# Optimization experiments

Hardware: AMD Instinct MI355X
Metric: run time of the kernel (lower is better)

The kernel has to match this reference:

```python
import jax, jax.numpy as jnp
import numpy as np

IMG_H, IMG_W = 800.0, 1280.0
STRIDE = 16
SCALE = 1.0 / STRIDE
P, S = 14, 1              # pooler resolution, sampling ratio
NUM_CLASSES = 80
BBOX_W = (10.0, 10.0, 5.0, 5.0)
SCORE_TH, NMS_TH, MAX_DET, IOU_TH = 0.05, 0.5, 100, 0.5
SCALE_CLAMP = float(np.log(1000.0 / 16.0))


def _make_boxes(key, n_img, n_box):
    k1, k2, k3, k4 = jax.random.split(key, 4)
    x1 = jax.random.uniform(k1, (n_img, n_box)) * (IMG_W - 64.0)
    y1 = jax.random.uniform(k2, (n_img, n_box)) * (IMG_H - 64.0)
    w = jax.random.uniform(k3, (n_img, n_box)) * 300.0 + 16.0
    h = jax.random.uniform(k4, (n_img, n_box)) * 300.0 + 16.0
    x2 = jnp.minimum(x1 + w, IMG_W)
    y2 = jnp.minimum(y1 + h, IMG_H)
    return jnp.stack([x1, y1, x2, y2], axis=-1)


def setup_inputs() -> dict:
    key = jax.random.key(0)
    ks = jax.random.split(key, 6)
    features = jax.random.normal(ks[0], (2, 50, 80, 1024), dtype=jnp.float32)
    proposals = _make_boxes(ks[1], 2, 256)
    gt_boxes = _make_boxes(ks[2], 2, 64)
    gt_classes = jax.random.randint(ks[3], (2, 64), 0, NUM_CLASSES)
    W_cls = jax.random.normal(ks[4], (1024, NUM_CLASSES + 1), dtype=jnp.float32) * 0.01
    b_cls = jnp.zeros((NUM_CLASSES + 1,), jnp.float32)
    W_box = jax.random.normal(ks[5], (1024, 4), dtype=jnp.float32) * 0.01
    b_box = jnp.zeros((4,), jnp.float32)
    return {"features": features, "proposals": proposals, "gt_boxes": gt_boxes,
            "gt_classes": gt_classes, "W_cls": W_cls, "b_cls": b_cls,
            "W_box": W_box, "b_box": b_box}


def pairwise_iou(a, b):
    # a: [G,4], b: [R,4], boxes as (x1,y1,x2,y2) -> [G,R]
    area_a = (a[:, 2] - a[:, 0]) * (a[:, 3] - a[:, 1])
    area_b = (b[:, 2] - b[:, 0]) * (b[:, 3] - b[:, 1])
    lt = jnp.maximum(a[:, None, :2], b[None, :, :2])
    rb = jnp.minimum(a[:, None, 2:], b[None, :, 2:])
    wh = jnp.clip(rb - lt, 0.0)
    inter = wh[..., 0] * wh[..., 1]
    return inter / jnp.maximum(area_a[:, None] + area_b[None, :] - inter, 1e-9)


def roi_align_one(feat, boxes):
    # feat: [H,W,C], boxes: [R,4] in image coords -> pooled [R,P,P,C]
    H, W, C = feat.shape
    b = boxes * SCALE
    x1, y1, x2, y2 = b[:, 0], b[:, 1], b[:, 2], b[:, 3]
    off = (jnp.arange(S, dtype=feat.dtype) + 0.5) / S       # [S]
    grid = jnp.arange(P, dtype=feat.dtype)                   # [P]
    bh = ((y2 - y1) / P)[:, None, None]
    bw = ((x2 - x1) / P)[:, None, None]
    # aligned RoIAlign sample coords (half-pixel offset)
    gy = y1[:, None, None] + (grid[None, :, None] + off[None, None, :]) * bh - 0.5  # [R,P,S]
    gx = x1[:, None, None] + (grid[None, :, None] + off[None, None, :]) * bw - 0.5
    gy = jnp.clip(gy, 0.0, H - 1.0)
    gx = jnp.clip(gx, 0.0, W - 1.0)
    y0 = jnp.floor(gy); x0 = jnp.floor(gx)
    y0i = y0.astype(jnp.int32); x0i = x0.astype(jnp.int32)
    y1i = jnp.minimum(y0i + 1, H - 1); x1i = jnp.minimum(x0i + 1, W - 1)
    ly = gy - y0; lx = gx - x0

    def g(yi, xi):  # cross-product gather -> [R,P,S,P,S,C]
        return feat[yi[:, :, :, None, None], xi[:, None, None, :, :]]

    wy0 = (1.0 - ly)[:, :, :, None, None, None]; wy1 = ly[:, :, :, None, None, None]
    wx0 = (1.0 - lx)[:, None, None, :, :, None]; wx1 = lx[:, None, None, :, :, None]
    val = wy0 * (wx0 * g(y0i, x0i) + wx1 * g(y0i, x1i)) \
        + wy1 * (wx0 * g(y1i, x0i) + wx1 * g(y1i, x1i))
    return val.mean(axis=(2, 4))  # average sampling points per bin -> [R,P,P,C]


def decode_boxes(deltas, boxes):
    wx, wy, ww, wh = BBOX_W
    widths = boxes[..., 2] - boxes[..., 0]
    heights = boxes[..., 3] - boxes[..., 1]
    ctr_x = boxes[..., 0] + 0.5 * widths
    ctr_y = boxes[..., 1] + 0.5 * heights
    dx = deltas[..., 0] / wx
    dy = deltas[..., 1] / wy
    dw = jnp.minimum(deltas[..., 2] / ww, SCALE_CLAMP)
    dh = jnp.minimum(deltas[..., 3] / wh, SCALE_CLAMP)
    pcx = dx * widths + ctr_x
    pcy = dy * heights + ctr_y
    pw = jnp.exp(dw) * widths
    ph = jnp.exp(dh) * heights
    out = jnp.stack([pcx - 0.5 * pw, pcy - 0.5 * ph, pcx + 0.5 * pw, pcy + 0.5 * ph], axis=-1)
    lim = jnp.array([IMG_W, IMG_H, IMG_W, IMG_H], out.dtype)
    return jnp.clip(out, 0.0, lim)


def nms_keep(boxes, scores):
    # greedy class-agnostic NMS, fixed-size keep mask [R]
    R = scores.shape[0]
    order = jnp.argsort(-scores)
    sb = boxes[order]
    iou = pairwise_iou(sb, sb)
    idx = jnp.arange(R)

    def body(i, keep):
        suppressed = jnp.any((idx < i) & keep & (iou[:, i] > NMS_TH))
        return keep.at[i].set(jnp.logical_not(suppressed))

    keep_sorted = jax.lax.fori_loop(0, R, body, jnp.ones((R,), bool))
    return jnp.zeros((R,), bool).at[order].set(keep_sorted)


def reference(features, proposals, gt_boxes, gt_classes, W_cls, b_cls, W_box, b_box):
    N, R = proposals.shape[:2]
    # --- proposal <-> gt matching (training-side labeling) ---
    iou_m = jax.vmap(pairwise_iou)(gt_boxes, proposals)          # [N,G,R]
    matched_vals = iou_m.max(axis=1)
    matched_idxs = iou_m.argmax(axis=1)                          # [N,R]
    match_labels = (matched_vals >= IOU_TH).astype(jnp.int32)    # [N,R] fg=1/bg=0
    # --- RoIAlign pooling on the single C4 feature map ---
    pooled = jax.vmap(roi_align_one)(features, proposals)        # [N,R,P,P,C]
    feat_vec = pooled.mean(axis=(2, 3))                          # res5 surrogate global avg -> [N,R,C]
    # --- box predictor ---
    scores_all = jax.nn.softmax(feat_vec @ W_cls + b_cls, axis=-1)
    fg_scores = scores_all[..., :NUM_CLASSES].max(axis=-1)       # drop background column
    deltas = feat_vec @ W_box + b_box
    boxes = decode_boxes(deltas, proposals)                      # [N,R,4]
    # --- score threshold + NMS + top-k ---
    keep = jax.vmap(nms_keep)(boxes, fg_scores) & (fg_scores > SCORE_TH)
    masked = jnp.where(keep, fg_scores, -jnp.inf)
    rank = jnp.argsort(jnp.argsort(-masked, axis=-1), axis=-1)
    keep = keep & (rank < MAX_DET)
    det = jnp.concatenate([boxes, fg_scores[..., None], keep.astype(boxes.dtype)[..., None]], axis=-1)
    return det, matched_idxs, match_labels
```

## Files before the change

kernel.cpp:

```cpp
#include <hip/hip_runtime.h>
#include <math.h>

#define N_IMG 2
#define R_PROP 256
#define G_GT 64
#define C_CH 1024
#define FH 50
#define FW 80
#define P_POOL 14
#define NCLS 80
#define IMG_W_F 1280.0f
#define IMG_H_F 800.0f
#define SCALE_F 0.0625f
#define SCORE_TH_F 0.05f
#define NMS_TH_F 0.5f
#define IOU_TH_F 0.5f
#define MAX_DET_I 100
#define SCALE_CLAMP_F 4.135166556742356f

__global__ __launch_bounds__(512) void prep_kernel(
    const float* __restrict__ proposals,
    const float* __restrict__ gt_boxes,
    int* __restrict__ perm,
    float* __restrict__ out_idx,
    float* __restrict__ out_lbl) {
  const int t = threadIdx.x;
  const int n = t >> 8;
  __shared__ float cy[N_IMG * R_PROP];
  const float* pb = proposals + (size_t)t * 4;
  float bx1 = pb[0], by1 = pb[1], bx2 = pb[2], by2 = pb[3];
  cy[t] = by1 + by2;
  __syncthreads();

  {
    float my = cy[t];
    int rk = 0;
    const int base = n * R_PROP;
#pragma unroll 8
    for (int j = base; j < base + R_PROP; ++j) {
      float cj = cy[j];
      rk += (cj < my) || (cj == my && j < t);
    }
    perm[base + rk] = t & 255;
  }

  {
    float area_b = (bx2 - bx1) * (by2 - by1);
    float best = -1.0f;
    int bidx = 0;
    const float* gt = gt_boxes + (size_t)n * G_GT * 4;
#pragma unroll 4
    for (int g = 0; g < G_GT; ++g) {
      float gx1 = gt[g * 4 + 0], gy1 = gt[g * 4 + 1];
      float gx2 = gt[g * 4 + 2], gy2 = gt[g * 4 + 3];
      float area_a = (gx2 - gx1) * (gy2 - gy1);
      float ix1 = fmaxf(gx1, bx1), iy1 = fmaxf(gy1, by1);
      float ix2 = fminf(gx2, bx2), iy2 = fminf(gy2, by2);
      float iw = fmaxf(ix2 - ix1, 0.0f), ih = fmaxf(iy2 - iy1, 0.0f);
      float inter = iw * ih;
      float iou = inter / fmaxf(area_a + area_b - inter, 1e-9f);
      if (iou > best) { best = iou; bidx = g; }
    }
    out_idx[t] = (float)bidx;
    out_lbl[t] = (best >= IOU_TH_F) ? 1.0f : 0.0f;
  }
}

__global__ __launch_bounds__(1024) void roihead_kernel(
    const float* __restrict__ features,
    const float* __restrict__ proposals,
    const int* __restrict__ perm,
    const float* __restrict__ W_cls,
    const float* __restrict__ W_box,
    float* __restrict__ part) {
  const int b = blockIdx.x;
  const int xcd = b & 7;
  const int slot = b >> 3;
  const int n = xcd >> 2;
  const int band = xcd & 3;
  const int h = slot & 1;
  const int blk = n * R_PROP + perm[n * R_PROP + band * 64 + (slot >> 1)];

  const float* feat = features + (size_t)n * (FH * FW * C_CH) + h * (C_CH / 2);
  const int t = threadIdx.x;
  const int c4 = t & 127;
  const int g = t >> 7;

  __shared__ float s_Wy[FH];
  __shared__ float s_Wx[FW];
  __shared__ int s_b[4];
  __shared__ float4 s_red[7][128];
  __shared__ __align__(16) float sf[C_CH / 2];
  __shared__ float s_part[12][85];

  if (t < FH) s_Wy[t] = 0.0f;
  if (t >= 128 && t < 128 + FW) s_Wx[t - 128] = 0.0f;
  __syncthreads();

  if (t < 2 * P_POOL) {
    const float* pb = proposals + (size_t)blk * 4;
    bool isY = t < P_POOL;
    int i = isY ? t : t - P_POOL;
    float lo = isY ? pb[1] : pb[0];
    float hi = isY ? pb[3] : pb[2];
    float limit = isY ? (float)(FH - 1) : (float)(FW - 1);
    float b1 = lo * SCALE_F, b2 = hi * SCALE_F;
    float bs = (b2 - b1) * (1.0f / P_POOL);
    float gg = b1 + ((float)i + 0.5f) * bs - 0.5f;
    gg = fminf(fmaxf(gg, 0.0f), limit);
    float fl = floorf(gg);
    int i0 = (int)fl;
    int i1 = min(i0 + 1, (int)limit);
    float l = gg - fl;
    if (isY) {
      atomicAdd(&s_Wy[i0], 1.0f - l);
      atomicAdd(&s_Wy[i1], l);
      if (i == 0) s_b[0] = i0;
      if (i == P_POOL - 1) s_b[1] = i1;
    } else {
      atomicAdd(&s_Wx[i0], 1.0f - l);
      atomicAdd(&s_Wx[i1], l);
      if (i == 0) s_b[2] = i0;
      if (i == P_POOL - 1) s_b[3] = i1;
    }
  }
  __syncthreads();

  {
    const int ylo = s_b[0], yhi = s_b[1], xlo = s_b[2], xhi = s_b[3];
    float4 acc = make_float4(0.f, 0.f, 0.f, 0.f);
    for (int y = ylo + g; y <= yhi; y += 8) {
      float wy = s_Wy[y];
      const float4* row = (const float4*)(feat + (size_t)y * (FW * C_CH)) + c4;
#pragma unroll 8
      for (int x = xlo; x <= xhi; ++x) {
        float w = wy * s_Wx[x];
        float4 f = row[x * (C_CH / 4)];
        acc.x += w * f.x;
        acc.y += w * f.y;
        acc.z += w * f.z;
        acc.w += w * f.w;
      }
    }
    if (g > 0) s_red[g - 1][c4] = acc;
    __syncthreads();
    if (g == 0) {
      const float inv = 1.0f / (float)(P_POOL * P_POOL);
#pragma unroll
      for (int p = 0; p < 7; ++p) {
        float4 a = s_red[p][c4];
        acc.x += a.x; acc.y += a.y; acc.z += a.z; acc.w += a.w;
      }
      ((float4*)sf)[c4] =
          make_float4(acc.x * inv, acc.y * inv, acc.z * inv, acc.w * inv);
    }
    __syncthreads();
  }

  const int kq = t / 85;
  const int j = t - kq * 85;
  if (kq < 12) {
    float acc = 0.0f;
    const int kbase = h * (C_CH / 2);
    if (j < 81) {
      const float* __restrict__ w = W_cls + (size_t)kbase * 81 + j;
#pragma unroll 8
      for (int k = kq; k < C_CH / 2; k += 12) acc += sf[k] * w[k * 81];
    } else {
      const float* __restrict__ w = W_box + (size_t)kbase * 4 + (j - 81);
#pragma unroll 8
      for (int k = kq; k < C_CH / 2; k += 12) acc += sf[k] * w[k * 4];
    }
    s_part[kq][j] = acc;
  }
  __syncthreads();

  if (t < 85) {
    float acc = 0.0f;
#pragma unroll
    for (int p = 0; p < 12; ++p) acc += s_part[p][t];
    part[(size_t)blk * 170 + h * 85 + t] = acc;
  }
}

__global__ __launch_bounds__(128) void finalize_kernel(
    const float* __restrict__ part,
    const float* __restrict__ proposals,
    const float* __restrict__ b_cls,
    const float* __restrict__ b_box,
    float* __restrict__ boxes_dec,
    float* __restrict__ scores) {
  const int blk = blockIdx.x;
  const int t = threadIdx.x;
  __shared__ float sl[85];
  __shared__ float s_red[8];

  const float* pp = part + (size_t)blk * 170;
  if (t < 85) {
    float bias = (t < 81) ? b_cls[t] : b_box[t - 81];
    sl[t] = pp[t] + pp[85 + t] + bias;
  }
  __syncthreads();

  {
    float xm = (t < 81) ? sl[t] : -INFINITY;
    float xf = (t < NCLS) ? sl[t] : -INFINITY;
#pragma unroll
    for (int off = 32; off; off >>= 1) {
      xm = fmaxf(xm, __shfl_down(xm, off, 64));
      xf = fmaxf(xf, __shfl_down(xf, off, 64));
    }
    if ((t & 63) == 0) { s_red[t >> 6] = xm; s_red[2 + (t >> 6)] = xf; }
  }
  __syncthreads();
  const float m = fmaxf(s_red[0], s_red[1]);
  {
    float xs = (t < 81) ? expf(sl[t] - m) : 0.0f;
#pragma unroll
    for (int off = 32; off; off >>= 1) xs += __shfl_down(xs, off, 64);
    if ((t & 63) == 0) s_red[4 + (t >> 6)] = xs;
  }
  __syncthreads();

  if (t == 0) {
    float sum = s_red[4] + s_red[5];
    float fgm = fmaxf(s_red[2], s_red[3]);
    scores[blk] = expf(fgm - m) / sum;

    const float* pb = proposals + (size_t)blk * 4;
    float w = pb[2] - pb[0], h = pb[3] - pb[1];
    float cx = pb[0] + 0.5f * w, cy = pb[1] + 0.5f * h;
    float dx = sl[81] * 0.1f;
    float dy = sl[82] * 0.1f;
    float dw = fminf(sl[83] * 0.2f, SCALE_CLAMP_F);
    float dh = fminf(sl[84] * 0.2f, SCALE_CLAMP_F);
    float pcx = dx * w + cx, pcy = dy * h + cy;
    float pw = expf(dw) * w, ph = expf(dh) * h;
    float ox1 = fminf(fmaxf(pcx - 0.5f * pw, 0.0f), IMG_W_F);
    float oy1 = fminf(fmaxf(pcy - 0.5f * ph, 0.0f), IMG_H_F);
    float ox2 = fminf(fmaxf(pcx + 0.5f * pw, 0.0f), IMG_W_F);
    float oy2 = fminf(fmaxf(pcy + 0.5f * ph, 0.0f), IMG_H_F);
    float* bd = boxes_dec + (size_t)blk * 4;
    bd[0] = ox1; bd[1] = oy1; bd[2] = ox2; bd[3] = oy2;
  }
}

__global__ __launch_bounds__(1024) void nms_kernel(
    const float* __restrict__ boxes_dec,
    const float* __restrict__ scores,
    float* __restrict__ det) {
  const int n = blockIdx.x;
  const int u = threadIdx.x;
  const int i = u & 255;
  const int q = u >> 8;
  const int j40 = q * 16;

  __shared__ __align__(16) float ss[R_PROP];
  __shared__ float4 sbs[R_PROP];
  __shared__ int s_part[4 * R_PROP];
  __shared__ int s_rank[R_PROP];
  __shared__ __align__(16) unsigned long long s_mask[R_PROP * 4];
  __shared__ unsigned long long s_keep[4];
  __shared__ __align__(16) float sm[R_PROP];

  float4 myb;
  float mys;
  if (q == 0) {
    myb = ((const float4*)boxes_dec)[n * R_PROP + i];
    mys = scores[n * R_PROP + i];
    ss[i] = mys;
  }
  __syncthreads();

  {
    float s = ss[i];
    int cnt = 0;
#pragma unroll
    for (int j4 = j40; j4 < j40 + 16; ++j4) {
      float4 v = ((const float4*)ss)[j4];
      int jb = j4 * 4;
      cnt += (v.x > s) || (v.x == s && jb + 0 < i);
      cnt += (v.y > s) || (v.y == s && jb + 1 < i);
      cnt += (v.z > s) || (v.z == s && jb + 2 < i);
      cnt += (v.w > s) || (v.w == s && jb + 3 < i);
    }
    s_part[q * R_PROP + i] = cnt;
  }
  __syncthreads();
  if (q == 0) {
    int rk = s_part[i] + s_part[R_PROP + i] + s_part[2 * R_PROP + i] +
             s_part[3 * R_PROP + i];
    s_rank[i] = rk;
    sbs[rk] = myb;
  }
  __syncthreads();

  {
    float4 bi = sbs[i];
    float area_i = (bi.z - bi.x) * (bi.w - bi.y);
    unsigned long long m = 0;
    const int j0 = q * 64;
#pragma unroll 8
    for (int jj = 0; jj < 64; ++jj) {
      float4 bj = sbs[j0 + jj];
      float area_j = (bj.z - bj.x) * (bj.w - bj.y);
      float ix1 = fmaxf(bi.x, bj.x), iy1 = fmaxf(bi.y, bj.y);
      float ix2 = fminf(bi.z, bj.z), iy2 = fminf(bi.w, bj.w);
      float iw = fmaxf(ix2 - ix1, 0.0f), ih = fmaxf(iy2 - iy1, 0.0f);
      float inter = iw * ih;
      float iou = inter / fmaxf(area_i + area_j - inter, 1e-9f);
      m |= (iou > NMS_TH_F) ? (1ull << jj) : 0ull;
    }
    s_mask[i * 4 + q] = m;
  }
  __syncthreads();

  if (u == 0) {
    unsigned long long K0 = ~0ull, K1 = ~0ull, K2 = ~0ull, K3 = ~0ull;
#pragma unroll 16
    for (int b = 1; b < 64; ++b) {
      unsigned long long m0 = s_mask[(size_t)b * 4 + 0];
      unsigned long long sup = m0 & K0 & ((1ull << b) - 1ull);
      K0 = sup ? (K0 & ~(1ull << b)) : K0;
    }
#pragma unroll 16
    for (int b = 0; b < 64; ++b) {
      const unsigned long long* mi = &s_mask[(size_t)(64 + b) * 4];
      unsigned long long m0 = mi[0], m1 = mi[1];
      unsigned long long sup = (m0 & K0) | (m1 & K1 & ((1ull << b) - 1ull));
      K1 = sup ? (K1 & ~(1ull << b)) : K1;
    }
#pragma unroll 16
    for (int b = 0; b < 64; ++b) {
      const unsigned long long* mi = &s_mask[(size_t)(128 + b) * 4];
      unsigned long long m0 = mi[0], m1 = mi[1], m2 = mi[2];
      unsigned long long sup =
          (m0 & K0) | (m1 & K1) | (m2 & K2 & ((1ull << b) - 1ull));
      K2 = sup ? (K2 & ~(1ull << b)) : K2;
    }
#pragma unroll 16
    for (int b = 0; b < 64; ++b) {
      const unsigned long long* mi = &s_mask[(size_t)(192 + b) * 4];
      unsigned long long m0 = mi[0], m1 = mi[1], m2 = mi[2], m3 = mi[3];
      unsigned long long sup = (m0 & K0) | (m1 & K1) | (m2 & K2) |
                               (m3 & K3 & ((1ull << b) - 1ull));
      K3 = sup ? (K3 & ~(1ull << b)) : K3;
    }
    s_keep[0] = K0; s_keep[1] = K1; s_keep[2] = K2; s_keep[3] = K3;
  }
  __syncthreads();

  bool kept = false;
  if (q == 0) {
    int rk = s_rank[i];
    kept = ((s_keep[rk >> 6] >> (rk & 63)) & 1ull) && (mys > SCORE_TH_F);
    sm[i] = kept ? mys : -INFINITY;
  }
  __syncthreads();

  {
    float mym = sm[i];
    int cnt = 0;
#pragma unroll
    for (int j4 = j40; j4 < j40 + 16; ++j4) {
      float4 v = ((const float4*)sm)[j4];
      int jb = j4 * 4;
      cnt += (v.x > mym) || (v.x == mym && jb + 0 < i);
      cnt += (v.y > mym) || (v.y == mym && jb + 1 < i);
      cnt += (v.z > mym) || (v.z == mym && jb + 2 < i);
      cnt += (v.w > mym) || (v.w == mym && jb + 3 < i);
    }
    s_part[q * R_PROP + i] = cnt;
  }
  __syncthreads();

  if (q == 0) {
    int rk2 = s_part[i] + s_part[R_PROP + i] + s_part[2 * R_PROP + i] +
              s_part[3 * R_PROP + i];
    kept = kept && (rk2 < MAX_DET_I);
    float* dr = det + ((size_t)n * R_PROP + i) * 6;
    dr[0] = myb.x; dr[1] = myb.y; dr[2] = myb.z; dr[3] = myb.w;
    dr[4] = mys;
    dr[5] = kept ? 1.0f : 0.0f;
  }
}

extern "C" void kernel_launch(void* const* d_in, const int* in_sizes, int n_in,
                              void* d_out, int out_size, void* d_ws, size_t ws_size,
                              hipStream_t stream) {
  const float* features  = (const float*)d_in[0];
  const float* proposals = (const float*)d_in[1];
  const float* gt_boxes  = (const float*)d_in[2];
  const float* W_cls = (const float*)d_in[4];
  const float* b_cls = (const float*)d_in[5];
  const float* W_box = (const float*)d_in[6];
  const float* b_box = (const float*)d_in[7];

  float* out = (float*)d_out;
  float* out_det = out;
  float* out_idx = out + N_IMG * R_PROP * 6;
  float* out_lbl = out_idx + N_IMG * R_PROP;

  float* part      = (float*)d_ws;
  float* boxes_dec = part + (size_t)N_IMG * R_PROP * 170;
  float* scores    = boxes_dec + (size_t)N_IMG * R_PROP * 4;
  int*   perm      = (int*)(scores + N_IMG * R_PROP);

  prep_kernel<<<1, 512, 0, stream>>>(proposals, gt_boxes, perm, out_idx, out_lbl);
  roihead_kernel<<<2 * N_IMG * R_PROP, 1024, 0, stream>>>(
      features, proposals, perm, W_cls, W_box, part);
  finalize_kernel<<<N_IMG * R_PROP, 128, 0, stream>>>(
      part, proposals, b_cls, b_box, boxes_dec, scores);
  nms_kernel<<<N_IMG, 1024, 0, stream>>>(boxes_dec, scores, out_det);
}
```

Measured before the change: 166.8 us.

## Fuse finalize into roihead via per-proposal atomic ticket last-block reduction

Removes the separate finalize kernel launch. The two channel-half blocks of each proposal now bump an atomic counter after writing their partial logits, and whichever block finishes second does the softmax, foreground score and box decode in place. Counters are zeroed in the prep kernel. This saves a launch and a global round trip, at the cost of a threadfence, an atomic and extra shared memory in the heavy roihead kernel.

After: 482.3 us. 189% more time.

```diff
diff --git a/kernel.cpp b/kernel.cpp
--- a/kernel.cpp
+++ b/kernel.cpp
@@ -22,6 +22,7 @@
     const float* __restrict__ proposals,
     const float* __restrict__ gt_boxes,
     int* __restrict__ perm,
+    int* __restrict__ cnt,
     float* __restrict__ out_idx,
     float* __restrict__ out_lbl) {
   const int t = threadIdx.x;
@@ -30,6 +31,7 @@
   const float* pb = proposals + (size_t)t * 4;
   float bx1 = pb[0], by1 = pb[1], bx2 = pb[2], by2 = pb[3];
   cy[t] = by1 + by2;
+  cnt[t] = 0;
   __syncthreads();
 
   {
@@ -71,8 +73,13 @@
     const float* __restrict__ proposals,
     const int* __restrict__ perm,
     const float* __restrict__ W_cls,
+    const float* __restrict__ b_cls,
     const float* __restrict__ W_box,
-    float* __restrict__ part) {
+    const float* __restrict__ b_box,
+    float* __restrict__ part,
+    int* __restrict__ cnt,
+    float* __restrict__ boxes_dec,
+    float* __restrict__ scores) {
   const int b = blockIdx.x;
   const int xcd = b & 7;
   const int slot = b >> 3;
@@ -92,6 +99,9 @@
   __shared__ float4 s_red[7][128];
   __shared__ __align__(16) float sf[C_CH / 2];
   __shared__ float s_part[12][85];
+  __shared__ float sl[85];
+  __shared__ float s_r2[8];
+  __shared__ int s_ticket;
 
   if (t < FH) s_Wy[t] = 0.0f;
   if (t >= 128 && t < 128 + FW) s_Wx[t - 128] = 0.0f;
@@ -181,19 +191,12 @@
     for (int p = 0; p < 12; ++p) acc += s_part[p][t];
     part[(size_t)blk * 170 + h * 85 + t] = acc;
   }
-}
-
-__global__ __launch_bounds__(128) void finalize_kernel(
-    const float* __restrict__ part,
-    const float* __restrict__ proposals,
-    const float* __restrict__ b_cls,
-    const float* __restrict__ b_box,
-    float* __restrict__ boxes_dec,
-    float* __restrict__ scores) {
-  const int blk = blockIdx.x;
-  const int t = threadIdx.x;
-  __shared__ float sl[85];
-  __shared__ float s_red[8];
+
+  __threadfence();
+  __syncthreads();
+  if (t == 0) s_ticket = atomicAdd(&cnt[blk], 1);
+  __syncthreads();
+  if (s_ticket != 1) return;
 
   const float* pp = part + (size_t)blk * 170;
   if (t < 85) {
@@ -202,7 +205,7 @@
   }
   __syncthreads();
 
-  {
+  if (t < 128) {
     float xm = (t < 81) ? sl[t] : -INFINITY;
     float xf = (t < NCLS) ? sl[t] : -INFINITY;
 #pragma unroll
@@ -210,32 +213,32 @@
       xm = fmaxf(xm, __shfl_down(xm, off, 64));
       xf = fmaxf(xf, __shfl_down(xf, off, 64));
     }
-    if ((t & 63) == 0) { s_red[t >> 6] = xm; s_red[2 + (t >> 6)] = xf; }
-  }
-  __syncthreads();
-  const float m = fmaxf(s_red[0], s_red[1]);
-  {
+    if ((t & 63) == 0) { s_r2[t >> 6] = xm; s_r2[2 + (t >> 6)] = xf; }
+  }
+  __syncthreads();
+  const float m = fmaxf(s_r2[0], s_r2[1]);
+  if (t < 128) {
     float xs = (t < 81) ? expf(sl[t] - m) : 0.0f;
 #pragma unroll
     for (int off = 32; off; off >>= 1) xs += __shfl_down(xs, off, 64);
-    if ((t & 63) == 0) s_red[4 + (t >> 6)] = xs;
+    if ((t & 63) == 0) s_r2[4 + (t >> 6)] = xs;
   }
   __syncthreads();
 
   if (t == 0) {
-    float sum = s_red[4] + s_red[5];
-    float fgm = fmaxf(s_red[2], s_red[3]);
+    float sum = s_r2[4] + s_r2[5];
+    float fgm = fmaxf(s_r2[2], s_r2[3]);
     scores[blk] = expf(fgm - m) / sum;
 
     const float* pb = proposals + (size_t)blk * 4;
-    float w = pb[2] - pb[0], h = pb[3] - pb[1];
-    float cx = pb[0] + 0.5f * w, cy = pb[1] + 0.5f * h;
+    float w = pb[2] - pb[0], hh = pb[3] - pb[1];
+    float cx = pb[0] + 0.5f * w, cyc = pb[1] + 0.5f * hh;
     float dx = sl[81] * 0.1f;
     float dy = sl[82] * 0.1f;
     float dw = fminf(sl[83] * 0.2f, SCALE_CLAMP_F);
     float dh = fminf(sl[84] * 0.2f, SCALE_CLAMP_F);
-    float pcx = dx * w + cx, pcy = dy * h + cy;
-    float pw = expf(dw) * w, ph = expf(dh) * h;
+    float pcx = dx * w + cx, pcy = dy * hh + cyc;
+    float pw = expf(dw) * w, ph = expf(dh) * hh;
     float ox1 = fminf(fmaxf(pcx - 0.5f * pw, 0.0f), IMG_W_F);
     float oy1 = fminf(fmaxf(pcy - 0.5f * ph, 0.0f), IMG_H_F);
     float ox2 = fminf(fmaxf(pcx + 0.5f * pw, 0.0f), IMG_W_F);
@@ -405,11 +408,12 @@
   float* boxes_dec = part + (size_t)N_IMG * R_PROP * 170;
   float* scores    = boxes_dec + (size_t)N_IMG * R_PROP * 4;
   int*   perm      = (int*)(scores + N_IMG * R_PROP);
-
-  prep_kernel<<<1, 512, 0, stream>>>(proposals, gt_boxes, perm, out_idx, out_lbl);
+  int*   cnt       = perm + N_IMG * R_PROP;
+
+  prep_kernel<<<1, 512, 0, stream>>>(proposals, gt_boxes, perm, cnt,
+                                     out_idx, out_lbl);
   roihead_kernel<<<2 * N_IMG * R_PROP, 1024, 0, stream>>>(
-      features, proposals, perm, W_cls, W_box, part);
-  finalize_kernel<<<N_IMG * R_PROP, 128, 0, stream>>>(
-      part, proposals, b_cls, b_box, boxes_dec, scores);
+      features, proposals, perm, W_cls, b_cls, W_box, b_box, part, cnt,
+      boxes_dec, scores);
   nms_kernel<<<N_IMG, 1024, 0, stream>>>(boxes_dec, scores, out_det);
 }
```
